# Kernel tuning notes

Hardware: AMD Instinct MI355X
Metric: run time of the kernel (lower is better)

## Reference

```python
import jax, jax.numpy as jnp
import numpy as np

S = 32          # input grid resolution
N = 2048        # active input voxels
C = 256         # in channels
CO = 128        # out channels
S2 = 2 * S      # upsampled resolution
M = 8 * N       # candidate child voxels
EPS = 1e-6


def setup_inputs() -> dict:
    key = jax.random.key(0)
    ks = jax.random.split(key, 8)
    # unique voxel coordinates (sparse occupancy)
    lin = jax.random.permutation(ks[0], S ** 3)[:N]
    coords = jnp.stack([lin // (S * S), (lin // S) % S, lin % S], axis=-1).astype(jnp.int32)
    sc = 0.05
    return {
        "feats": jax.random.normal(ks[1], (N, C), jnp.float32),
        "norm1_w": 1.0 + 0.1 * jax.random.normal(ks[2], (C,), jnp.float32),
        "norm1_b": 0.1 * jax.random.normal(ks[3], (C,), jnp.float32),
        "subdiv_w": sc * jax.random.normal(ks[4], (C, 8), jnp.float32),
        "subdiv_b": jnp.zeros((8,), jnp.float32),
        "conv1_w": sc * jax.random.normal(ks[5], (27, C, CO), jnp.float32),
        "conv1_b": jnp.zeros((CO,), jnp.float32),
        "conv2_w": sc * jax.random.normal(ks[6], (27, CO, CO), jnp.float32),
        "conv2_b": jnp.zeros((CO,), jnp.float32),
        "skip_w": sc * jax.random.normal(ks[7], (C, CO), jnp.float32),
        "skip_b": jnp.zeros((CO,), jnp.float32),
        "coords": coords,
    }


def _layernorm(x, w=None, b=None):
    # LayerNorm32: fp32 math, eps=1e-6
    m = jnp.mean(x, axis=-1, keepdims=True)
    v = jnp.var(x, axis=-1, keepdims=True)
    y = (x - m) * jax.lax.rsqrt(v + EPS)
    if w is not None:
        y = y * w + b
    return y


def _sparse_conv(feats, nidx, w, b):
    # submanifold 3x3x3 sparse conv: gather 27 neighbors, contract.
    # nidx: [M,27] with sentinel M pointing at a zero row.
    pad = jnp.concatenate([feats, jnp.zeros((1, feats.shape[1]), feats.dtype)], axis=0)
    g = pad[nidx]                                   # [M, 27, Cin]
    return jnp.einsum('nkc,kcd->nd', g, w) + b


def _forward(feats, norm1_w, norm1_b, subdiv_w, subdiv_b, conv1_w, conv1_b,
             conv2_w, conv2_b, skip_w, skip_b, coords):
    # subdiv prediction (SparseLinear C -> 8)
    subdiv = feats @ subdiv_w + subdiv_b            # [N, 8]
    # norm1 + silu
    h = jax.nn.silu(_layernorm(feats, norm1_w, norm1_b))
    # sparse upsample x2 with octree subdivision mask
    mask = (subdiv > 0).reshape(-1)                 # [M]
    j = jnp.arange(8, dtype=jnp.int32)
    offs8 = jnp.stack([(j >> 2) & 1, (j >> 1) & 1, j & 1], axis=-1)  # [8,3]
    cc = (coords[:, None, :] * 2 + offs8[None]).reshape(-1, 3)        # [M,3]
    h_c = jnp.where(mask[:, None], jnp.repeat(h, 8, axis=0), 0.0)     # [M,C]
    x_c = jnp.where(mask[:, None], jnp.repeat(feats, 8, axis=0), 0.0)
    # neighbor lookup grid (padded by 1; default M -> zero feature row)
    grid = jnp.full((S2 + 2, S2 + 2, S2 + 2), M, jnp.int32)
    grid = grid.at[cc[:, 0] + 1, cc[:, 1] + 1, cc[:, 2] + 1].set(
        jnp.arange(M, dtype=jnp.int32))
    d = jnp.arange(-1, 2, dtype=jnp.int32)
    offs27 = jnp.stack(jnp.meshgrid(d, d, d, indexing='ij'), axis=-1).reshape(27, 3)
    nc = cc[:, None, :] + 1 + offs27[None]          # [M,27,3]
    nidx = grid[nc[..., 0], nc[..., 1], nc[..., 2]] # [M,27]
    # conv1 -> norm2 (no affine) -> silu -> conv2
    h1 = jax.nn.silu(_layernorm(_sparse_conv(h_c, nidx, conv1_w, conv1_b)))
    h2 = _sparse_conv(h1, nidx, conv2_w, conv2_b)
    # residual with linear skip; mask out non-subdivided children
    out = (h2 + x_c @ skip_w + skip_b) * mask[:, None].astype(h2.dtype)
    return out, subdiv


def reference(feats, norm1_w, norm1_b, subdiv_w, subdiv_b, conv1_w, conv1_b,
              conv2_w, conv2_b, skip_w, skip_b, coords):
    return _forward(feats, norm1_w, norm1_b, subdiv_w, subdiv_b, conv1_w,
                    conv1_b, conv2_w, conv2_b, skip_w, skip_b, coords)
```

## Files before the change

kernel.cpp:

```cpp
#include <hip/hip_runtime.h>
#include <cstdint>
#include <cstddef>

constexpr int N  = 2048;
constexpr int C  = 256;
constexpr int CO = 128;
constexpr int M  = 16384;
constexpr int G  = 66;
constexpr int KP2 = 4;
constexpr int KCHUNK2 = 7;
constexpr int UW = 27 * CO;
constexpr float EPS = 1e-6f;

using bf8 = __attribute__((ext_vector_type(8))) short;
using f4  = __attribute__((ext_vector_type(4))) float;

static __device__ __forceinline__ unsigned short f2bf(float f) {
  unsigned u = __float_as_uint(f);
  u += 0x7fffu + ((u >> 16) & 1u);
  return (unsigned short)(u >> 16);
}
static __device__ __forceinline__ float bf2f(unsigned short s) {
  return __uint_as_float((unsigned)s << 16);
}

__global__ void k_prep(int* __restrict__ grid, unsigned short* __restrict__ h,
                       unsigned short* __restrict__ h1,
                       const float* __restrict__ c1w, unsigned short* __restrict__ w1t,
                       const float* __restrict__ c2w, unsigned short* __restrict__ w2t) {
  int i = blockIdx.x * 256 + threadIdx.x;
  if (i < G * G * G) grid[i] = M;
  if (i < C)  h[(size_t)N * C + i] = 0;
  if (i < CO) h1[(size_t)M * CO + i] = 0;
  if (i < 27 * C * CO) {
    int c = i % C;
    int rest = i / C;
    int o = rest % CO;
    int k = rest / CO;
    w1t[i] = f2bf(c1w[((size_t)(k * C + c)) * CO + o]);
  }
  if (i < 27 * CO * CO) {
    int c = i % CO;
    int rest = i / CO;
    int o = rest % CO;
    int k = rest / CO;
    w2t[i] = f2bf(c2w[((size_t)(k * CO + c)) * CO + o]);
  }
}

__global__ __launch_bounds__(256) void k_rownorm(
    const float* __restrict__ feats, const float* __restrict__ n1w,
    const float* __restrict__ n1b, const float* __restrict__ sdw,
    const float* __restrict__ sdb, float* __restrict__ out_subdiv,
    unsigned short* __restrict__ h, int* __restrict__ pidx,
    float* __restrict__ maskf, const int* __restrict__ coords,
    int* __restrict__ grid) {
  int n = blockIdx.x, t = threadIdx.x;
  float x = feats[(size_t)n * C + t];
  float4 w0 = *(const float4*)(sdw + t * 8);
  float4 w1 = *(const float4*)(sdw + t * 8 + 4);
  float v[10] = {x * w0.x, x * w0.y, x * w0.z, x * w0.w,
                 x * w1.x, x * w1.y, x * w1.z, x * w1.w, x, x * x};
#pragma unroll
  for (int mk = 1; mk < 64; mk <<= 1) {
#pragma unroll
    for (int j = 0; j < 10; ++j) v[j] += __shfl_xor(v[j], mk, 64);
  }
  __shared__ float red[4][10];
  int wave = t >> 6, lane = t & 63;
  if (lane == 0) {
#pragma unroll
    for (int j = 0; j < 10; ++j) red[wave][j] = v[j];
  }
  __syncthreads();
  float sums[10];
#pragma unroll
  for (int j = 0; j < 10; ++j)
    sums[j] = red[0][j] + red[1][j] + red[2][j] + red[3][j];
  float mean = sums[8] / (float)C;
  float var  = sums[9] / (float)C - mean * mean;
  float rstd = rsqrtf(var + EPS);
  if (t < 8) {
    float sd = sums[t] + sdb[t];
    out_subdiv[(size_t)n * 8 + t] = sd;
    bool mk = sd > 0.f;
    pidx[n * 8 + t]  = mk ? n : N;
    maskf[n * 8 + t] = mk ? 1.f : 0.f;
    int xx = coords[n * 3 + 0] * 2 + ((t >> 2) & 1) + 1;
    int yy = coords[n * 3 + 1] * 2 + ((t >> 1) & 1) + 1;
    int zz = coords[n * 3 + 2] * 2 + (t & 1) + 1;
    grid[(xx * G + yy) * G + zz] = n * 8 + t;
  }
  float y  = (x - mean) * rstd * n1w[t] + n1b[t];
  float sl = y / (1.f + __expf(-y));
  h[(size_t)n * C + t] = f2bf(sl);
}

__global__ void k_nidx(const int* __restrict__ coords, const int* __restrict__ grid,
                       const int* __restrict__ pidx, int* __restrict__ nidxt,
                       int* __restrict__ g1t) {
  int idx = blockIdx.x * 256 + threadIdx.x;
  if (idx >= M * 27) return;
  int m = idx & (M - 1);
  int k = idx >> 14;
  int p = m >> 3, j = m & 7;
  int dx = k / 9 - 1;
  int dy = (k / 3) % 3 - 1;
  int dz = k % 3 - 1;
  int x = coords[p * 3 + 0] * 2 + ((j >> 2) & 1) + 1 + dx;
  int y = coords[p * 3 + 1] * 2 + ((j >> 1) & 1) + 1 + dy;
  int z = coords[p * 3 + 2] * 2 + (j & 1) + 1 + dz;
  int gv = grid[(x * G + y) * G + z];
  nidxt[idx] = gv;
  g1t[idx] = (gv == M) ? N : pidx[gv];
}

__global__ __launch_bounds__(256) void k_skip(const float* __restrict__ feats,
                                              const float* __restrict__ skw,
                                              const float* __restrict__ skb,
                                              float* __restrict__ s) {
  __shared__ float tile[32][36];
  int t = threadIdx.x;
  int rb = (blockIdx.x >> 1) * 32;
  int ob = (blockIdx.x & 1) * 64;
  int o = ob + (t & 63);
  int rg = (t >> 6) * 8;
  float acc[8] = {0, 0, 0, 0, 0, 0, 0, 0};
  for (int cb = 0; cb < C; cb += 32) {
    __syncthreads();
    int row = t >> 3, cc = (t & 7) * 4;
    *(float4*)&tile[row][cc] =
        *(const float4*)(feats + (size_t)(rb + row) * C + cb + cc);
    __syncthreads();
    for (int c = 0; c < 32; ++c) {
      float wv = skw[(size_t)(cb + c) * CO + o];
#pragma unroll
      for (int r = 0; r < 8; ++r) acc[r] += tile[rg + r][c] * wv;
    }
  }
  float bv = skb[o];
#pragma unroll
  for (int r = 0; r < 8; ++r) s[(size_t)(rb + rg + r) * CO + o] = acc[r] + bv;
}

template <int CIN, int NCB>
__global__ __launch_bounds__(256, 3) void k_dgemm(
    const unsigned short* __restrict__ src, const unsigned short* __restrict__ wt,
    float* __restrict__ U) {
  __shared__ unsigned short sA[2][128 * 32];
  __shared__ unsigned short sB[2][128 * 32];
  const int t = threadIdx.x;
  const int w = t >> 6, lane = t & 63;
  const int quad = lane >> 4, ln = lane & 15;
  const int m0 = blockIdx.x * 128;
  const int k = blockIdx.y;
  const int rh = (w >> 1) * 64, ch = (w & 1) * 64;

  const int row2 = t >> 1;
  const int c0 = (t & 1) * 2;
  const int x3 = (row2 >> 1) & 3;
  const int wsl0 = row2 * 32 + ((c0) ^ x3) * 8;
  const int wsl1 = row2 * 32 + ((c0 + 1) ^ x3) * 8;

  const unsigned short* pa_base = src + (size_t)(m0 + row2) * CIN + c0 * 8;
  const unsigned short* pb_base =
      wt + ((size_t)k * CO + row2) * CIN + c0 * 8;

  bf8 ra0, ra1, rb0, rb1;
  auto loadreg = [&](int s) {
    const unsigned short* pa = pa_base + s * 32;
    const unsigned short* pb = pb_base + s * 32;
    ra0 = *(const bf8*)(pa);
    ra1 = *(const bf8*)(pa + 8);
    rb0 = *(const bf8*)(pb);
    rb1 = *(const bf8*)(pb + 8);
  };
  auto writelds = [&](int buf) {
    *(bf8*)(sA[buf] + wsl0) = ra0;
    *(bf8*)(sA[buf] + wsl1) = ra1;
    *(bf8*)(sB[buf] + wsl0) = rb0;
    *(bf8*)(sB[buf] + wsl1) = rb1;
  };

  f4 acc[16];
  f4 zero = {0.f, 0.f, 0.f, 0.f};
#pragma unroll
  for (int i = 0; i < 16; ++i) acc[i] = zero;

  const int slot = (quad ^ ((ln >> 1) & 3)) * 8;

  loadreg(0);
  writelds(0);
  for (int s = 0; s < NCB; ++s) {
    const bool have = (s + 1 < NCB);
    if (have) loadreg(s + 1);
    __syncthreads();
    const unsigned short* pa = sA[s & 1];
    const unsigned short* pb = sB[s & 1];
    bf8 av[4], bv[4];
#pragma unroll
    for (int ti = 0; ti < 4; ++ti)
      av[ti] = *(const bf8*)(pa + (rh + ti * 16 + ln) * 32 + slot);
#pragma unroll
    for (int tj = 0; tj < 4; ++tj)
      bv[tj] = *(const bf8*)(pb + (ch + tj * 16 + ln) * 32 + slot);
#pragma unroll
    for (int ti = 0; ti < 4; ++ti)
#pragma unroll
      for (int tj = 0; tj < 4; ++tj)
        acc[ti * 4 + tj] = __builtin_amdgcn_mfma_f32_16x16x32_bf16(
            av[ti], bv[tj], acc[ti * 4 + tj], 0, 0, 0);
    if (have) writelds((s + 1) & 1);
  }

#pragma unroll
  for (int ti = 0; ti < 4; ++ti) {
    int mrow = rh + ti * 16 + quad * 4;
#pragma unroll
    for (int tj = 0; tj < 4; ++tj) {
      int co = ch + tj * 16 + ln;
#pragma unroll
      for (int rr = 0; rr < 4; ++rr)
        U[(size_t)(m0 + mrow + rr) * UW + k * CO + co] = acc[ti * 4 + tj][rr];
    }
  }
}

__global__ __launch_bounds__(256) void k_g1sum(
    const float* __restrict__ U, const int* __restrict__ g1t,
    const float* __restrict__ b1, unsigned short* __restrict__ h1) {
  int wave = threadIdx.x >> 6, lane = threadIdx.x & 63;
  int m = blockIdx.x * 4 + wave;
  float a0 = b1[2 * lane], a1 = b1[2 * lane + 1];
#pragma unroll
  for (int k = 0; k < 27; ++k) {
    int g = g1t[k * M + m];
    if (g < N) {
      float2 v = *(const float2*)(U + (size_t)g * UW + k * CO + 2 * lane);
      a0 += v.x; a1 += v.y;
    }
  }
  float sum = a0 + a1, sq = a0 * a0 + a1 * a1;
#pragma unroll
  for (int mk = 1; mk < 64; mk <<= 1) {
    sum += __shfl_xor(sum, mk, 64);
    sq  += __shfl_xor(sq, mk, 64);
  }
  float mean = sum / (float)CO;
  float var  = sq / (float)CO - mean * mean;
  float rstd = rsqrtf(var + EPS);
  float y0 = (a0 - mean) * rstd;
  float y1 = (a1 - mean) * rstd;
  float s0 = y0 / (1.f + __expf(-y0));
  float s1 = y1 / (1.f + __expf(-y1));
  *(ushort2*)(h1 + (size_t)m * CO + 2 * lane) = ushort2{f2bf(s0), f2bf(s1)};
}

template <int CIN, int NCB, int KCH>
__global__ __launch_bounds__(256, 3) void k_conv(
    const unsigned short* __restrict__ src, const int* __restrict__ gt,
    const unsigned short* __restrict__ wt, unsigned short* __restrict__ part) {
  __shared__ unsigned short sA[2][128 * 32];
  __shared__ unsigned short sB[2][128 * 32];
  const int t = threadIdx.x;
  const int w = t >> 6, lane = t & 63;
  const int quad = lane >> 4, ln = lane & 15;
  const int m0 = blockIdx.x * 128;
  const int kpart = blockIdx.y;
  const int k0 = kpart * KCH;
  const int nk = min(KCH, 27 - k0);
  const int nstage = nk * NCB;
  const int rh = (w >> 1) * 64, ch = (w & 1) * 64;

  const int row2 = t >> 1;
  const int c0 = (t & 1) * 2;
  const int x3 = (row2 >> 1) & 3;
  const int wsl0 = row2 * 32 + ((c0) ^ x3) * 8;
  const int wsl1 = row2 * 32 + ((c0 + 1) ^ x3) * 8;

  int ga[KCH];
#pragma unroll
  for (int kk = 0; kk < KCH; ++kk)
    ga[kk] = (kk < nk) ? gt[(size_t)(k0 + kk) * M + m0 + row2] : 0;

  bf8 ra0, ra1, rb0, rb1;
  auto loadreg = [&](int s) {
    const int kk = s / NCB;
    const int cb = s - kk * NCB;
    const unsigned short* pa = src + (size_t)ga[kk] * CIN + cb * 32 + c0 * 8;
    const unsigned short* pb =
        wt + ((size_t)(k0 + kk) * CO + row2) * CIN + cb * 32 + c0 * 8;
    ra0 = *(const bf8*)(pa);
    ra1 = *(const bf8*)(pa + 8);
    rb0 = *(const bf8*)(pb);
    rb1 = *(const bf8*)(pb + 8);
  };
  auto writelds = [&](int buf) {
    *(bf8*)(sA[buf] + wsl0) = ra0;
    *(bf8*)(sA[buf] + wsl1) = ra1;
    *(bf8*)(sB[buf] + wsl0) = rb0;
    *(bf8*)(sB[buf] + wsl1) = rb1;
  };

  f4 acc[16];
  f4 zero = {0.f, 0.f, 0.f, 0.f};
#pragma unroll
  for (int i = 0; i < 16; ++i) acc[i] = zero;

  const int slot = (quad ^ ((ln >> 1) & 3)) * 8;

  loadreg(0);
  writelds(0);
  for (int s = 0; s < nstage; ++s) {
    const bool have = (s + 1 < nstage);
    if (have) loadreg(s + 1);
    __syncthreads();
    const unsigned short* pa = sA[s & 1];
    const unsigned short* pb = sB[s & 1];
    bf8 av[4], bv[4];
#pragma unroll
    for (int ti = 0; ti < 4; ++ti)
      av[ti] = *(const bf8*)(pa + (rh + ti * 16 + ln) * 32 + slot);
#pragma unroll
    for (int tj = 0; tj < 4; ++tj)
      bv[tj] = *(const bf8*)(pb + (ch + tj * 16 + ln) * 32 + slot);
#pragma unroll
    for (int ti = 0; ti < 4; ++ti)
#pragma unroll
      for (int tj = 0; tj < 4; ++tj)
        acc[ti * 4 + tj] = __builtin_amdgcn_mfma_f32_16x16x32_bf16(
            av[ti], bv[tj], acc[ti * 4 + tj], 0, 0, 0);
    if (have) writelds((s + 1) & 1);
  }

  unsigned short* pp = part + ((size_t)kpart * M + m0) * CO;
#pragma unroll
  for (int ti = 0; ti < 4; ++ti) {
    int mrow = rh + ti * 16 + quad * 4;
#pragma unroll
    for (int tj = 0; tj < 4; ++tj) {
      int co = ch + tj * 16 + ln;
#pragma unroll
      for (int rr = 0; rr < 4; ++rr)
        pp[(size_t)(mrow + rr) * CO + co] = f2bf(acc[ti * 4 + tj][rr]);
    }
  }
}

__global__ __launch_bounds__(256) void k_r2(const unsigned short* __restrict__ p,
                                            const float* __restrict__ bias,
                                            const float* __restrict__ sres,
                                            const float* __restrict__ maskf,
                                            float* __restrict__ out) {
  int i = blockIdx.x * 256 + threadIdx.x;
  int m = i >> 5;
  int o4 = (i & 31) * 4;
  float4 acc = *(const float4*)(bias + o4);
#pragma unroll
  for (int q = 0; q < KP2; ++q) {
    ushort4 a = *(const ushort4*)(p + ((size_t)q * M + m) * CO + o4);
    acc.x += bf2f(a.x); acc.y += bf2f(a.y);
    acc.z += bf2f(a.z); acc.w += bf2f(a.w);
  }
  float4 s = *(const float4*)(sres + (size_t)(m >> 3) * CO + o4);
  float mk = maskf[m];
  float4 r;
  r.x = (acc.x + s.x) * mk;
  r.y = (acc.y + s.y) * mk;
  r.z = (acc.z + s.z) * mk;
  r.w = (acc.w + s.w) * mk;
  *(float4*)(out + (size_t)m * CO + o4) = r;
}

extern "C" void kernel_launch(void* const* d_in, const int* in_sizes, int n_in,
                              void* d_out, int out_size, void* d_ws, size_t ws_size,
                              hipStream_t stream) {
  const float* feats = (const float*)d_in[0];
  const float* n1w   = (const float*)d_in[1];
  const float* n1b   = (const float*)d_in[2];
  const float* sdw   = (const float*)d_in[3];
  const float* sdb   = (const float*)d_in[4];
  const float* c1w   = (const float*)d_in[5];
  const float* c1b   = (const float*)d_in[6];
  const float* c2w   = (const float*)d_in[7];
  const float* c2b   = (const float*)d_in[8];
  const float* skw   = (const float*)d_in[9];
  const float* skb   = (const float*)d_in[10];
  const int* coords  = (const int*)d_in[11];
  float* out = (float*)d_out;

  char* ws = (char*)d_ws;
  size_t off = 0;
  auto alloc = [&](size_t bytes) -> char* {
    char* p = ws + off;
    off += (bytes + 255) & ~(size_t)255;
    return p;
  };
  unsigned short* h    = (unsigned short*)alloc((size_t)(N + 1) * C * 2);
  unsigned short* h1   = (unsigned short*)alloc((size_t)(M + 1) * CO * 2);
  int*   grid  = (int*)alloc((size_t)G * G * G * 4);
  int*   nidxt = (int*)alloc((size_t)27 * M * 4);
  int*   g1t   = (int*)alloc((size_t)27 * M * 4);
  int*   pidx  = (int*)alloc((size_t)M * 4);
  float* maskf = (float*)alloc((size_t)M * 4);
  float* sres  = (float*)alloc((size_t)N * CO * 4);
  unsigned short* w1t = (unsigned short*)alloc((size_t)27 * CO * C * 2);
  unsigned short* w2t = (unsigned short*)alloc((size_t)27 * CO * CO * 2);
  float* U = (float*)alloc((size_t)N * UW * 4);
  unsigned short* pc  = (unsigned short*)alloc((size_t)KP2 * M * CO * 2);

  k_prep<<<(27 * C * CO + 255) / 256, 256, 0, stream>>>(grid, h, h1, c1w, w1t,
                                                        c2w, w2t);
  k_rownorm<<<N, 256, 0, stream>>>(feats, n1w, n1b, sdw, sdb,
                                   out + (size_t)M * CO, h, pidx, maskf,
                                   coords, grid);
  k_nidx<<<(M * 27 + 255) / 256, 256, 0, stream>>>(coords, grid, pidx, nidxt, g1t);
  k_skip<<<128, 256, 0, stream>>>(feats, skw, skb, sres);

  k_dgemm<C, 8><<<dim3(N / 128, 27), 256, 0, stream>>>(h, w1t, U);
  k_g1sum<<<M / 4, 256, 0, stream>>>(U, g1t, c1b, h1);

  k_conv<CO, 4, KCHUNK2><<<dim3(M / 128, KP2), 256, 0, stream>>>(h1, nidxt, w2t, pc);
  k_r2<<<M * CO / 4 / 256, 256, 0, stream>>>(pc, c2b, sres, maskf, out);
}
```

Before: 179.9 us.

## Compact active child voxels and skip masked rows in conv2

Assigns each subdivided child a compact index with an atomic counter, builds a compacted neighbor table, and has conv2 blocks beyond the active count exit early. The final combine kernel reads partials through the compact index and writes zeros for masked rows. The K split changes from 4 parts of 7 offsets to 7 parts of 4 offsets, and the weight transpose in k_prep now goes through a shared-memory tiled transpose. The atomic ordering makes row placement nondeterministic, which leaves results unchanged but adds an atomic in rownorm.

New measurement: 190.1 us. 5.7% more time.

```diff
diff --git a/kernel.cpp b/kernel.cpp
--- a/kernel.cpp
+++ b/kernel.cpp
@@ -7,8 +7,8 @@
 constexpr int CO = 128;
 constexpr int M  = 16384;
 constexpr int G  = 66;
-constexpr int KP2 = 4;
-constexpr int KCHUNK2 = 7;
+constexpr int KP2 = 7;
+constexpr int KCHUNK2 = 4;
 constexpr int UW = 27 * CO;
 constexpr float EPS = 1e-6f;
 
@@ -24,28 +24,56 @@
   return __uint_as_float((unsigned)s << 16);
 }
 
-__global__ void k_prep(int* __restrict__ grid, unsigned short* __restrict__ h,
-                       unsigned short* __restrict__ h1,
-                       const float* __restrict__ c1w, unsigned short* __restrict__ w1t,
-                       const float* __restrict__ c2w, unsigned short* __restrict__ w2t) {
-  int i = blockIdx.x * 256 + threadIdx.x;
+__global__ __launch_bounds__(256) void k_prep(
+    int* __restrict__ grid, unsigned short* __restrict__ h,
+    unsigned short* __restrict__ h1, const float* __restrict__ c1w,
+    unsigned short* __restrict__ w1t, const float* __restrict__ c2w,
+    unsigned short* __restrict__ w2t, int* __restrict__ nidxtc,
+    int* __restrict__ nact) {
+  const int b = blockIdx.x, t = threadIdx.x;
+  if (b < 864) {
+    __shared__ unsigned short tile[32][33];
+    int k = b >> 5, r = b & 31;
+    int cb = (r >> 2) * 32, ob = (r & 3) * 32;
+    int lr = t >> 5, lc = t & 31;
+#pragma unroll
+    for (int it = 0; it < 4; ++it) {
+      int c = cb + lr + 8 * it, o = ob + lc;
+      tile[lr + 8 * it][lc] = f2bf(c1w[((size_t)k * C + c) * CO + o]);
+    }
+    __syncthreads();
+#pragma unroll
+    for (int it = 0; it < 4; ++it) {
+      int o = ob + lr + 8 * it;
+      w1t[((size_t)k * CO + o) * C + cb + lc] = tile[lc][lr + 8 * it];
+    }
+    return;
+  }
+  if (b < 1296) {
+    __shared__ unsigned short tile[32][33];
+    int ti = b - 864;
+    int k = ti >> 4, r = ti & 15;
+    int cb = (r >> 2) * 32, ob = (r & 3) * 32;
+    int lr = t >> 5, lc = t & 31;
+#pragma unroll
+    for (int it = 0; it < 4; ++it) {
+      int c = cb + lr + 8 * it, o = ob + lc;
+      tile[lr + 8 * it][lc] = f2bf(c2w[((size_t)k * CO + c) * CO + o]);
+    }
+    __syncthreads();
+#pragma unroll
+    for (int it = 0; it < 4; ++it) {
+      int o = ob + lr + 8 * it;
+      w2t[((size_t)k * CO + o) * CO + cb + lc] = tile[lc][lr + 8 * it];
+    }
+    return;
+  }
+  int i = (b - 1296) * 256 + t;
   if (i < G * G * G) grid[i] = M;
+  nidxtc[i] = M;
   if (i < C)  h[(size_t)N * C + i] = 0;
   if (i < CO) h1[(size_t)M * CO + i] = 0;
-  if (i < 27 * C * CO) {
-    int c = i % C;
-    int rest = i / C;
-    int o = rest % CO;
-    int k = rest / CO;
-    w1t[i] = f2bf(c1w[((size_t)(k * C + c)) * CO + o]);
-  }
-  if (i < 27 * CO * CO) {
-    int c = i % CO;
-    int rest = i / CO;
-    int o = rest % CO;
-    int k = rest / CO;
-    w2t[i] = f2bf(c2w[((size_t)(k * CO + c)) * CO + o]);
-  }
+  if (i == 0) *nact = 0;
 }
 
 __global__ __launch_bounds__(256) void k_rownorm(
@@ -53,8 +81,8 @@
     const float* __restrict__ n1b, const float* __restrict__ sdw,
     const float* __restrict__ sdb, float* __restrict__ out_subdiv,
     unsigned short* __restrict__ h, int* __restrict__ pidx,
-    float* __restrict__ maskf, const int* __restrict__ coords,
-    int* __restrict__ grid) {
+    int* __restrict__ inv, int* __restrict__ nact,
+    const int* __restrict__ coords, int* __restrict__ grid) {
   int n = blockIdx.x, t = threadIdx.x;
   float x = feats[(size_t)n * C + t];
   float4 w0 = *(const float4*)(sdw + t * 8);
@@ -84,12 +112,13 @@
     float sd = sums[t] + sdb[t];
     out_subdiv[(size_t)n * 8 + t] = sd;
     bool mk = sd > 0.f;
-    pidx[n * 8 + t]  = mk ? n : N;
-    maskf[n * 8 + t] = mk ? 1.f : 0.f;
+    int m = n * 8 + t;
+    pidx[m] = mk ? n : N;
+    inv[m] = mk ? atomicAdd(nact, 1) : -1;
     int xx = coords[n * 3 + 0] * 2 + ((t >> 2) & 1) + 1;
     int yy = coords[n * 3 + 1] * 2 + ((t >> 1) & 1) + 1;
     int zz = coords[n * 3 + 2] * 2 + (t & 1) + 1;
-    grid[(xx * G + yy) * G + zz] = n * 8 + t;
+    grid[(xx * G + yy) * G + zz] = m;
   }
   float y  = (x - mean) * rstd * n1w[t] + n1b[t];
   float sl = y / (1.f + __expf(-y));
@@ -97,8 +126,8 @@
 }
 
 __global__ void k_nidx(const int* __restrict__ coords, const int* __restrict__ grid,
-                       const int* __restrict__ pidx, int* __restrict__ nidxt,
-                       int* __restrict__ g1t) {
+                       const int* __restrict__ pidx, const int* __restrict__ inv,
+                       int* __restrict__ g1t, int* __restrict__ nidxtc) {
   int idx = blockIdx.x * 256 + threadIdx.x;
   if (idx >= M * 27) return;
   int m = idx & (M - 1);
@@ -111,8 +140,9 @@
   int y = coords[p * 3 + 1] * 2 + ((j >> 1) & 1) + 1 + dy;
   int z = coords[p * 3 + 2] * 2 + (j & 1) + 1 + dz;
   int gv = grid[(x * G + y) * G + z];
-  nidxt[idx] = gv;
   g1t[idx] = (gv == M) ? N : pidx[gv];
+  int ci = inv[m];
+  if (ci >= 0) nidxtc[(size_t)k * M + ci] = gv;
 }
 
 __global__ __launch_bounds__(256) void k_skip(const float* __restrict__ feats,
@@ -259,13 +289,15 @@
 template <int CIN, int NCB, int KCH>
 __global__ __launch_bounds__(256, 3) void k_conv(
     const unsigned short* __restrict__ src, const int* __restrict__ gt,
-    const unsigned short* __restrict__ wt, unsigned short* __restrict__ part) {
+    const unsigned short* __restrict__ wt, unsigned short* __restrict__ part,
+    const int* __restrict__ nact) {
+  const int m0 = blockIdx.x * 128;
+  if (m0 >= *nact) return;
   __shared__ unsigned short sA[2][128 * 32];
   __shared__ unsigned short sB[2][128 * 32];
   const int t = threadIdx.x;
   const int w = t >> 6, lane = t & 63;
   const int quad = lane >> 4, ln = lane & 15;
-  const int m0 = blockIdx.x * 128;
   const int kpart = blockIdx.y;
   const int k0 = kpart * KCH;
   const int nk = min(KCH, 27 - k0);
@@ -350,25 +382,27 @@
 __global__ __launch_bounds__(256) void k_r2(const unsigned short* __restrict__ p,
                                             const float* __restrict__ bias,
                                             const float* __restrict__ sres,
-                                            const float* __restrict__ maskf,
+                                            const int* __restrict__ inv,
                                             float* __restrict__ out) {
   int i = blockIdx.x * 256 + threadIdx.x;
   int m = i >> 5;
   int o4 = (i & 31) * 4;
-  float4 acc = *(const float4*)(bias + o4);
-#pragma unroll
-  for (int q = 0; q < KP2; ++q) {
-    ushort4 a = *(const ushort4*)(p + ((size_t)q * M + m) * CO + o4);
-    acc.x += bf2f(a.x); acc.y += bf2f(a.y);
-    acc.z += bf2f(a.z); acc.w += bf2f(a.w);
-  }
-  float4 s = *(const float4*)(sres + (size_t)(m >> 3) * CO + o4);
-  float mk = maskf[m];
-  float4 r;
-  r.x = (acc.x + s.x) * mk;
-  r.y = (acc.y + s.y) * mk;
-  r.z = (acc.z + s.z) * mk;
-  r.w = (acc.w + s.w) * mk;
+  int ci = inv[m];
+  float4 r = {0.f, 0.f, 0.f, 0.f};
+  if (ci >= 0) {
+    float4 acc = *(const float4*)(bias + o4);
+#pragma unroll
+    for (int q = 0; q < KP2; ++q) {
+      ushort4 a = *(const ushort4*)(p + ((size_t)q * M + ci) * CO + o4);
+      acc.x += bf2f(a.x); acc.y += bf2f(a.y);
+      acc.z += bf2f(a.z); acc.w += bf2f(a.w);
+    }
+    float4 s = *(const float4*)(sres + (size_t)(m >> 3) * CO + o4);
+    r.x = acc.x + s.x;
+    r.y = acc.y + s.y;
+    r.z = acc.z + s.z;
+    r.w = acc.w + s.w;
+  }
   *(float4*)(out + (size_t)m * CO + o4) = r;
 }
 
@@ -398,28 +432,31 @@
   };
   unsigned short* h    = (unsigned short*)alloc((size_t)(N + 1) * C * 2);
   unsigned short* h1   = (unsigned short*)alloc((size_t)(M + 1) * CO * 2);
-  int*   grid  = (int*)alloc((size_t)G * G * G * 4);
-  int*   nidxt = (int*)alloc((size_t)27 * M * 4);
-  int*   g1t   = (int*)alloc((size_t)27 * M * 4);
-  int*   pidx  = (int*)alloc((size_t)M * 4);
-  float* maskf = (float*)alloc((size_t)M * 4);
-  float* sres  = (float*)alloc((size_t)N * CO * 4);
+  int*   grid   = (int*)alloc((size_t)G * G * G * 4);
+  int*   nidxtc = (int*)alloc((size_t)27 * M * 4);
+  int*   g1t    = (int*)alloc((size_t)27 * M * 4);
+  int*   pidx   = (int*)alloc((size_t)M * 4);
+  int*   inv    = (int*)alloc((size_t)M * 4);
+  int*   nact   = (int*)alloc(256);
+  float* sres   = (float*)alloc((size_t)N * CO * 4);
   unsigned short* w1t = (unsigned short*)alloc((size_t)27 * CO * C * 2);
   unsigned short* w2t = (unsigned short*)alloc((size_t)27 * CO * CO * 2);
   float* U = (float*)alloc((size_t)N * UW * 4);
   unsigned short* pc  = (unsigned short*)alloc((size_t)KP2 * M * CO * 2);
 
-  k_prep<<<(27 * C * CO + 255) / 256, 256, 0, stream>>>(grid, h, h1, c1w, w1t,
-                                                        c2w, w2t);
+  k_prep<<<3024, 256, 0, stream>>>(grid, h, h1, c1w, w1t, c2w, w2t, nidxtc,
+                                   nact);
   k_rownorm<<<N, 256, 0, stream>>>(feats, n1w, n1b, sdw, sdb,
-                                   out + (size_t)M * CO, h, pidx, maskf,
+                                   out + (size_t)M * CO, h, pidx, inv, nact,
                                    coords, grid);
-  k_nidx<<<(M * 27 + 255) / 256, 256, 0, stream>>>(coords, grid, pidx, nidxt, g1t);
+  k_nidx<<<(M * 27 + 255) / 256, 256, 0, stream>>>(coords, grid, pidx, inv,
+                                                   g1t, nidxtc);
   k_skip<<<128, 256, 0, stream>>>(feats, skw, skb, sres);
 
   k_dgemm<C, 8><<<dim3(N / 128, 27), 256, 0, stream>>>(h, w1t, U);
   k_g1sum<<<M / 4, 256, 0, stream>>>(U, g1t, c1b, h1);
 
-  k_conv<CO, 4, KCHUNK2><<<dim3(M / 128, KP2), 256, 0, stream>>>(h1, nidxt, w2t, pc);
-  k_r2<<<M * CO / 4 / 256, 256, 0, stream>>>(pc, c2b, sres, maskf, out);
-}
+  k_conv<CO, 4, KCHUNK2><<<dim3(M / 128, KP2), 256, 0, stream>>>(h1, nidxtc,
+                                                                 w2t, pc, nact);
+  k_r2<<<M * CO / 4 / 256, 256, 0, stream>>>(pc, c2b, sres, inv, out);
+}
```

## Compact active child voxels so conv2 only computes rows kept by the mask

Applied to the files above, without the earlier changes.

Assigns each subdivided child a compact index via an atomic counter and builds a compacted neighbor table for those children only. The conv2 kernel exits early for blocks beyond the active count, and the final reduction reads partial sums by compact index, writing zeros for masked-out children. This avoids the conv2 GEMM on rows the mask discards anyway, at the cost of an atomic per child, an extra fill of the compacted index table, and a nondeterministic row order in the partial buffer.

Measured after the change: 193.1 us. 1.07x slower.

```diff
diff --git a/kernel.cpp b/kernel.cpp
--- a/kernel.cpp
+++ b/kernel.cpp
@@ -27,11 +27,14 @@
 __global__ void k_prep(int* __restrict__ grid, unsigned short* __restrict__ h,
                        unsigned short* __restrict__ h1,
                        const float* __restrict__ c1w, unsigned short* __restrict__ w1t,
-                       const float* __restrict__ c2w, unsigned short* __restrict__ w2t) {
+                       const float* __restrict__ c2w, unsigned short* __restrict__ w2t,
+                       int* __restrict__ nidxtc, int* __restrict__ nact) {
   int i = blockIdx.x * 256 + threadIdx.x;
   if (i < G * G * G) grid[i] = M;
+  if (i < 27 * M) nidxtc[i] = M;
   if (i < C)  h[(size_t)N * C + i] = 0;
   if (i < CO) h1[(size_t)M * CO + i] = 0;
+  if (i == 0) *nact = 0;
   if (i < 27 * C * CO) {
     int c = i % C;
     int rest = i / C;
@@ -53,8 +56,8 @@
     const float* __restrict__ n1b, const float* __restrict__ sdw,
     const float* __restrict__ sdb, float* __restrict__ out_subdiv,
     unsigned short* __restrict__ h, int* __restrict__ pidx,
-    float* __restrict__ maskf, const int* __restrict__ coords,
-    int* __restrict__ grid) {
+    int* __restrict__ inv, int* __restrict__ nact,
+    const int* __restrict__ coords, int* __restrict__ grid) {
   int n = blockIdx.x, t = threadIdx.x;
   float x = feats[(size_t)n * C + t];
   float4 w0 = *(const float4*)(sdw + t * 8);
@@ -84,12 +87,13 @@
     float sd = sums[t] + sdb[t];
     out_subdiv[(size_t)n * 8 + t] = sd;
     bool mk = sd > 0.f;
-    pidx[n * 8 + t]  = mk ? n : N;
-    maskf[n * 8 + t] = mk ? 1.f : 0.f;
+    int m = n * 8 + t;
+    pidx[m] = mk ? n : N;
+    inv[m] = mk ? atomicAdd(nact, 1) : -1;
     int xx = coords[n * 3 + 0] * 2 + ((t >> 2) & 1) + 1;
     int yy = coords[n * 3 + 1] * 2 + ((t >> 1) & 1) + 1;
     int zz = coords[n * 3 + 2] * 2 + (t & 1) + 1;
-    grid[(xx * G + yy) * G + zz] = n * 8 + t;
+    grid[(xx * G + yy) * G + zz] = m;
   }
   float y  = (x - mean) * rstd * n1w[t] + n1b[t];
   float sl = y / (1.f + __expf(-y));
@@ -97,8 +101,8 @@
 }
 
 __global__ void k_nidx(const int* __restrict__ coords, const int* __restrict__ grid,
-                       const int* __restrict__ pidx, int* __restrict__ nidxt,
-                       int* __restrict__ g1t) {
+                       const int* __restrict__ pidx, const int* __restrict__ inv,
+                       int* __restrict__ g1t, int* __restrict__ nidxtc) {
   int idx = blockIdx.x * 256 + threadIdx.x;
   if (idx >= M * 27) return;
   int m = idx & (M - 1);
@@ -111,8 +115,9 @@
   int y = coords[p * 3 + 1] * 2 + ((j >> 1) & 1) + 1 + dy;
   int z = coords[p * 3 + 2] * 2 + (j & 1) + 1 + dz;
   int gv = grid[(x * G + y) * G + z];
-  nidxt[idx] = gv;
   g1t[idx] = (gv == M) ? N : pidx[gv];
+  int ci = inv[m];
+  if (ci >= 0) nidxtc[(size_t)k * M + ci] = gv;
 }
 
 __global__ __launch_bounds__(256) void k_skip(const float* __restrict__ feats,
@@ -259,13 +264,15 @@
 template <int CIN, int NCB, int KCH>
 __global__ __launch_bounds__(256, 3) void k_conv(
     const unsigned short* __restrict__ src, const int* __restrict__ gt,
-    const unsigned short* __restrict__ wt, unsigned short* __restrict__ part) {
+    const unsigned short* __restrict__ wt, unsigned short* __restrict__ part,
+    const int* __restrict__ nact) {
+  const int m0 = blockIdx.x * 128;
+  if (m0 >= *nact) return;
   __shared__ unsigned short sA[2][128 * 32];
   __shared__ unsigned short sB[2][128 * 32];
   const int t = threadIdx.x;
   const int w = t >> 6, lane = t & 63;
   const int quad = lane >> 4, ln = lane & 15;
-  const int m0 = blockIdx.x * 128;
   const int kpart = blockIdx.y;
   const int k0 = kpart * KCH;
   const int nk = min(KCH, 27 - k0);
@@ -350,25 +357,27 @@
 __global__ __launch_bounds__(256) void k_r2(const unsigned short* __restrict__ p,
                                             const float* __restrict__ bias,
                                             const float* __restrict__ sres,
-                                            const float* __restrict__ maskf,
+                                            const int* __restrict__ inv,
                                             float* __restrict__ out) {
   int i = blockIdx.x * 256 + threadIdx.x;
   int m = i >> 5;
   int o4 = (i & 31) * 4;
-  float4 acc = *(const float4*)(bias + o4);
-#pragma unroll
-  for (int q = 0; q < KP2; ++q) {
-    ushort4 a = *(const ushort4*)(p + ((size_t)q * M + m) * CO + o4);
-    acc.x += bf2f(a.x); acc.y += bf2f(a.y);
-    acc.z += bf2f(a.z); acc.w += bf2f(a.w);
-  }
-  float4 s = *(const float4*)(sres + (size_t)(m >> 3) * CO + o4);
-  float mk = maskf[m];
-  float4 r;
-  r.x = (acc.x + s.x) * mk;
-  r.y = (acc.y + s.y) * mk;
-  r.z = (acc.z + s.z) * mk;
-  r.w = (acc.w + s.w) * mk;
+  int ci = inv[m];
+  float4 r = {0.f, 0.f, 0.f, 0.f};
+  if (ci >= 0) {
+    float4 acc = *(const float4*)(bias + o4);
+#pragma unroll
+    for (int q = 0; q < KP2; ++q) {
+      ushort4 a = *(const ushort4*)(p + ((size_t)q * M + ci) * CO + o4);
+      acc.x += bf2f(a.x); acc.y += bf2f(a.y);
+      acc.z += bf2f(a.z); acc.w += bf2f(a.w);
+    }
+    float4 s = *(const float4*)(sres + (size_t)(m >> 3) * CO + o4);
+    r.x = acc.x + s.x;
+    r.y = acc.y + s.y;
+    r.z = acc.z + s.z;
+    r.w = acc.w + s.w;
+  }
   *(float4*)(out + (size_t)m * CO + o4) = r;
 }
 
@@ -398,28 +407,31 @@
   };
   unsigned short* h    = (unsigned short*)alloc((size_t)(N + 1) * C * 2);
   unsigned short* h1   = (unsigned short*)alloc((size_t)(M + 1) * CO * 2);
-  int*   grid  = (int*)alloc((size_t)G * G * G * 4);
-  int*   nidxt = (int*)alloc((size_t)27 * M * 4);
-  int*   g1t   = (int*)alloc((size_t)27 * M * 4);
-  int*   pidx  = (int*)alloc((size_t)M * 4);
-  float* maskf = (float*)alloc((size_t)M * 4);
-  float* sres  = (float*)alloc((size_t)N * CO * 4);
+  int*   grid   = (int*)alloc((size_t)G * G * G * 4);
+  int*   nidxtc = (int*)alloc((size_t)27 * M * 4);
+  int*   g1t    = (int*)alloc((size_t)27 * M * 4);
+  int*   pidx   = (int*)alloc((size_t)M * 4);
+  int*   inv    = (int*)alloc((size_t)M * 4);
+  int*   nact   = (int*)alloc(256);
+  float* sres   = (float*)alloc((size_t)N * CO * 4);
   unsigned short* w1t = (unsigned short*)alloc((size_t)27 * CO * C * 2);
   unsigned short* w2t = (unsigned short*)alloc((size_t)27 * CO * CO * 2);
   float* U = (float*)alloc((size_t)N * UW * 4);
   unsigned short* pc  = (unsigned short*)alloc((size_t)KP2 * M * CO * 2);
 
   k_prep<<<(27 * C * CO + 255) / 256, 256, 0, stream>>>(grid, h, h1, c1w, w1t,
-                                                        c2w, w2t);
+                                                        c2w, w2t, nidxtc, nact);
   k_rownorm<<<N, 256, 0, stream>>>(feats, n1w, n1b, sdw, sdb,
-                                   out + (size_t)M * CO, h, pidx, maskf,
+                                   out + (size_t)M * CO, h, pidx, inv, nact,
                                    coords, grid);
-  k_nidx<<<(M * 27 + 255) / 256, 256, 0, stream>>>(coords, grid, pidx, nidxt, g1t);
+  k_nidx<<<(M * 27 + 255) / 256, 256, 0, stream>>>(coords, grid, pidx, inv,
+                                                   g1t, nidxtc);
   k_skip<<<128, 256, 0, stream>>>(feats, skw, skb, sres);
 
   k_dgemm<C, 8><<<dim3(N / 128, 27), 256, 0, stream>>>(h, w1t, U);
   k_g1sum<<<M / 4, 256, 0, stream>>>(U, g1t, c1b, h1);
 
-  k_conv<CO, 4, KCHUNK2><<<dim3(M / 128, KP2), 256, 0, stream>>>(h1, nidxt, w2t, pc);
-  k_r2<<<M * CO / 4 / 256, 256, 0, stream>>>(pc, c2b, sres, maskf, out);
-}
+  k_conv<CO, 4, KCHUNK2><<<dim3(M / 128, KP2), 256, 0, stream>>>(h1, nidxtc,
+                                                                 w2t, pc, nact);
+  k_r2<<<M * CO / 4 / 256, 256, 0, stream>>>(pc, c2b, sres, inv, out);
+}
```
